# Kernel tuning notes

Measured on AMD Instinct MI355X. Metric: run time of the kernel, lower is better.

## Reference

```python
import jax, jax.numpy as jnp
import numpy as np


def setup_inputs() -> dict:
    key = jax.random.key(0)
    ks = jax.random.split(key, 7)
    B, N, D = 32, 512, 64
    H = D // 2
    return {
        "receiver": jax.random.normal(ks[0], (B, N, D), dtype=jnp.float32),
        "attendant": jax.random.normal(ks[1], (B, N, D), dtype=jnp.float32),
        "adj_mask": jax.random.uniform(ks[2], (B, N, N), dtype=jnp.float32),
        "w_q": jax.random.normal(ks[3], (D, H), dtype=jnp.float32) * (1.0 / np.sqrt(D)),
        "w_k": jax.random.normal(ks[4], (D, H), dtype=jnp.float32) * (1.0 / np.sqrt(D)),
        "bias": jax.random.normal(ks[5], (H,), dtype=jnp.float32) * 0.1,
        "a": jax.random.normal(ks[6], (H,), dtype=jnp.float32) * 0.1,
    }


def reference(receiver, attendant, adj_mask, w_q, w_k, bias, a):
    # keys: [B,N,H], queries: [B,N,H]
    keys = receiver @ w_k
    queries = attendant @ w_q
    # additive (GAT-style) scores: broadcast-add -> tanh -> dot with a
    # e_act: [B, N, M, H]  (N from keys, M from queries, matching torch unsqueeze(-3)/(-2))
    e_act = jnp.tanh(queries[:, None, :, :] + keys[:, :, None, :] + bias)
    e_scores = jnp.einsum("bnmh,h->bnm", e_act, a)
    # masked projection: adj @ scores @ adj
    att = jnp.einsum("bnk,bkm->bnm", adj_mask, e_scores)
    att = jnp.einsum("bnk,bkm->bnm", att, adj_mask)
    return att
```

## Files before the change

kernel.cpp:

```cpp
#include <hip/hip_runtime.h>

#define GN 512
#define HH 32
#define DD 64

typedef float v4f __attribute__((ext_vector_type(4)));
typedef unsigned int v4u __attribute__((ext_vector_type(4)));
typedef u_int32_t u32;
typedef u32 v2u __attribute__((ext_vector_type(2)));
typedef __bf16 v8bf __attribute__((ext_vector_type(8)));

__device__ __forceinline__ u32 f2bf(float f) {
  u32 u = __builtin_bit_cast(u32, f);
  return (u + 0x7fffu + ((u >> 16) & 1u)) >> 16;
}
__device__ __forceinline__ u32 pack2(float a, float b) {
  return f2bf(a) | (f2bf(b) << 16);
}

#define GLOAD16(g, l)                                                              \
  __builtin_amdgcn_global_load_lds((const __attribute__((address_space(1))) u32*)(g), \
                                   (__attribute__((address_space(3))) u32*)(l), 16, 0, 0)
#define VMCNT0 asm volatile("s_waitcnt vmcnt(0)" ::: "memory")

__global__ __launch_bounds__(256) void kq_kernel(const float* __restrict__ rec,
                                                 const float* __restrict__ att,
                                                 const float* __restrict__ wq,
                                                 const float* __restrict__ wk,
                                                 const float* __restrict__ bias,
                                                 float* __restrict__ ekbuf,
                                                 float* __restrict__ eqbuf) {
  __shared__ float rr[512], ra[512];
  int tid = threadIdx.x;
  size_t base = (size_t)blockIdx.x * 8;
  const float* gr = rec + base * DD;
  const float* ga = att + base * DD;
  rr[tid] = gr[tid]; rr[tid + 256] = gr[tid + 256];
  ra[tid] = ga[tid]; ra[tid + 256] = ga[tid + 256];
  __syncthreads();
  int r = tid >> 5, h = tid & 31;
  float sk = bias[h], sq = 0.f;
  const float* rrow = &rr[r * DD];
  const float* arow = &ra[r * DD];
#pragma unroll 8
  for (int d = 0; d < DD; ++d) {
    sk += rrow[d] * wk[d * HH + h];
    sq += arow[d] * wq[d * HH + h];
  }
  const float C = 2.8853900817779268f;
  ekbuf[(base + r) * HH + h] = __builtin_exp2f(C * sk);
  eqbuf[(base + r) * HH + h] = __builtin_exp2f(C * sq);
}

__global__ __launch_bounds__(256) void prep2_kernel(const float* __restrict__ adj,
                                                    const float* __restrict__ ek,
                                                    const float* __restrict__ eq,
                                                    const float* __restrict__ avec,
                                                    unsigned short* __restrict__ adjT,
                                                    unsigned short* __restrict__ adjBF,
                                                    unsigned short* __restrict__ Et) {
  __shared__ __align__(16) float smem[4608];
  int tid = threadIdx.x;
  int bid = blockIdx.x;
  int type = bid % 5, grp = bid / 5;

  if (type < 4) {
    float (*klt)[68] = (float (*)[68])smem;
    float (*ql)[36] = (float (*)[36])&smem[2176];
    int e = grp * 4 + type;
    int b = e >> 6, rem = e & 63;
    int n0 = (rem & 7) * 64, m0 = (rem >> 3) * 64;

    const float* kb = ek + ((size_t)b * GN + n0) * HH;
    const float* qb = eq + ((size_t)b * GN + m0) * HH;
    int sr = tid >> 3, sp = tid & 7;
    v4f rk0 = *(const v4f*)(kb + sr * HH + sp * 4);
    v4f rq0 = *(const v4f*)(qb + sr * HH + sp * 4);
    v4f rk1 = *(const v4f*)(kb + (sr + 32) * HH + sp * 4);
    v4f rq1 = *(const v4f*)(qb + (sr + 32) * HH + sp * 4);
    *(v4f*)&ql[sr][sp * 4] = rq0;
    *(v4f*)&ql[sr + 32][sp * 4] = rq1;
#pragma unroll
    for (int ee = 0; ee < 4; ++ee) {
      klt[sp * 4 + ee][sr] = rk0[ee];
      klt[sp * 4 + ee][sr + 32] = rk1[ee];
    }

    float a2s[HH];
    float asum = 0.f;
#pragma unroll
    for (int h = 0; h < HH; ++h) {
      float av = avec[h];
      a2s[h] = 2.0f * av;
      asum += av;
    }
    __syncthreads();

    int mg = tid >> 4, ng = tid & 15;
    v4f acc[4];
#pragma unroll
    for (int i = 0; i < 4; ++i) acc[i] = (v4f){0.f, 0.f, 0.f, 0.f};

#pragma unroll
    for (int h4 = 0; h4 < 8; ++h4) {
      v4f kv[4], qv[4];
#pragma unroll
      for (int ee = 0; ee < 4; ++ee) kv[ee] = *(const v4f*)&klt[h4 * 4 + ee][4 * ng];
#pragma unroll
      for (int i = 0; i < 4; ++i) qv[i] = *(const v4f*)&ql[mg + 16 * i][h4 * 4];
      float a0 = a2s[h4 * 4 + 0], a1 = a2s[h4 * 4 + 1];
      float a2 = a2s[h4 * 4 + 2], a3 = a2s[h4 * 4 + 3];
#pragma unroll
      for (int i = 0; i < 4; ++i) {
        v4f f0 = kv[0] * qv[i][0] + 1.0f;
        v4f f1 = kv[1] * qv[i][1] + 1.0f;
        v4f f2 = kv[2] * qv[i][2] + 1.0f;
        v4f f3 = kv[3] * qv[i][3] + 1.0f;
        v4f den0 = f0 * f1, den1 = f2 * f3;
        v4f num0 = a0 * f1 + a1 * f0;
        v4f num1 = a2 * f3 + a3 * f2;
        v4f r0, r1;
#pragma unroll
        for (int ee = 0; ee < 4; ++ee) {
          r0[ee] = __builtin_amdgcn_rcpf(den0[ee]);
          r1[ee] = __builtin_amdgcn_rcpf(den1[ee]);
        }
        acc[i] += num0 * r0;
        acc[i] += num1 * r1;
      }
    }
#pragma unroll
    for (int i = 0; i < 4; ++i) {
      v4f s = asum - acc[i];
      v2u p = {pack2(s[0], s[1]), pack2(s[2], s[3])};
      *(v2u*)(Et + ((size_t)b * GN + m0 + mg + 16 * i) * GN + n0 + 4 * ng) = p;
    }
  } else {
    float (*t)[65] = (float (*)[65])smem;
#pragma unroll 1
    for (int l = 0; l < 4; ++l) {
      int tt = grp * 4 + l;
      int b = tt >> 6, rem = tt & 63;
      int c0 = (rem & 7) * 64, r0 = (rem >> 3) * 64;
      const float* ab = adj + (size_t)b * GN * GN;
      unsigned short* ob = adjT + (size_t)b * GN * GN;
      unsigned short* of = adjBF + (size_t)b * GN * GN;
#pragma unroll
      for (int k = 0; k < 4; ++k) {
        int v = tid + k * 256;
        int row = v >> 4, seg = v & 15;
        v4f f = *(const v4f*)(ab + (size_t)(r0 + row) * GN + c0 + seg * 4);
        t[row][seg * 4 + 0] = f[0];
        t[row][seg * 4 + 1] = f[1];
        t[row][seg * 4 + 2] = f[2];
        t[row][seg * 4 + 3] = f[3];
        v2u p = {pack2(f[0], f[1]), pack2(f[2], f[3])};
        *(v2u*)(of + (size_t)(r0 + row) * GN + c0 + seg * 4) = p;
      }
      __syncthreads();
      {
        int c = tid >> 2;
        int rs = (tid & 3) * 16;
        v4u p0, p1;
#pragma unroll
        for (int j = 0; j < 4; ++j) {
          p0[j] = pack2(t[rs + 2 * j][c], t[rs + 2 * j + 1][c]);
          p1[j] = pack2(t[rs + 8 + 2 * j][c], t[rs + 9 + 2 * j][c]);
        }
        unsigned short* dst = ob + (size_t)(c0 + c) * GN + r0 + rs;
        *(v4u*)dst = p0;
        *(v4u*)(dst + 8) = p1;
      }
      __syncthreads();
    }
  }
}

#define SWZ(r, s) ((s) ^ ((r) & 7))

template <bool OUTF32>
__global__ __launch_bounds__(256) void gemm_bt(const unsigned short* __restrict__ A,
                                               const unsigned short* __restrict__ Bt,
                                               void* __restrict__ Cv) {
  __shared__ unsigned short At[2][128 * 64];
  __shared__ unsigned short Bs[2][128 * 64];
  int bid = blockIdx.x;
  int swz = (bid & 7) * 64 + (bid >> 3);
  int b = swz >> 4;
  int row0 = ((swz >> 2) & 3) * 128;
  int col0 = (swz & 3) * 128;
  int tid = threadIdx.x, lane = tid & 63, wave = tid >> 6;
  int wr = wave >> 1, wc = wave & 1;
  const unsigned short* Ab = A + (size_t)b * GN * GN;
  const unsigned short* Bb = Bt + (size_t)b * GN * GN;

  v4f acc[4][4];
#pragma unroll
  for (int i = 0; i < 4; ++i)
#pragma unroll
    for (int j = 0; j < 4; ++j) acc[i][j] = (v4f){0.f, 0.f, 0.f, 0.f};

  int cc_r[4], cc_s[4];
#pragma unroll
  for (int i = 0; i < 4; ++i) {
    int c = i * 256 + tid;
    cc_r[i] = c >> 3;
    cc_s[i] = SWZ(c >> 3, c & 7);
  }

#define STAGE(buf, kt)                                                                   \
  {                                                                                      \
    _Pragma("unroll") for (int i = 0; i < 4; ++i) {                                      \
      const unsigned short* ga = Ab + (size_t)(row0 + cc_r[i]) * GN + (kt)*64 + cc_s[i] * 8; \
      const unsigned short* gb = Bb + (size_t)(col0 + cc_r[i]) * GN + (kt)*64 + cc_s[i] * 8; \
      GLOAD16(ga, (char*)&At[buf][0] + (i * 256 + wave * 64) * 16);                      \
      GLOAD16(gb, (char*)&Bs[buf][0] + (i * 256 + wave * 64) * 16);                      \
    }                                                                                    \
  }

#define COMPUTE(buf)                                                                     \
  {                                                                                      \
    int lr = lane & 15, s16 = lane >> 4;                                                 \
    _Pragma("unroll") for (int h = 0; h < 2; ++h) {                                      \
      int sl = h * 4 + s16;                                                              \
      v8bf af[4], bfv[4];                                                                \
      _Pragma("unroll") for (int i = 0; i < 4; ++i) {                                    \
        int r = wr * 64 + i * 16 + lr;                                                   \
        af[i] = *(const v8bf*)&At[buf][r * 64 + SWZ(r, sl) * 8];                         \
      }                                                                                  \
      _Pragma("unroll") for (int j = 0; j < 4; ++j) {                                    \
        int r = wc * 64 + j * 16 + lr;                                                   \
        bfv[j] = *(const v8bf*)&Bs[buf][r * 64 + SWZ(r, sl) * 8];                        \
      }                                                                                  \
      _Pragma("unroll") for (int i = 0; i < 4; ++i)                                      \
          _Pragma("unroll") for (int j = 0; j < 4; ++j) acc[i][j] =                      \
          __builtin_amdgcn_mfma_f32_16x16x32_bf16(af[i], bfv[j], acc[i][j], 0, 0, 0);    \
    }                                                                                    \
  }

  STAGE(0, 0);
  VMCNT0;
  __builtin_amdgcn_s_barrier();
#pragma unroll
  for (int kt = 0; kt < 7; ++kt) {
    int cur = kt & 1;
    STAGE(cur ^ 1, kt + 1);
    COMPUTE(cur);
    VMCNT0;
    __builtin_amdgcn_s_barrier();
  }
  COMPUTE(1);

  int lc = lane & 15;
  int lrow4 = (lane >> 4) * 4;
#pragma unroll
  for (int i = 0; i < 4; ++i) {
#pragma unroll
    for (int j = 0; j < 4; ++j) {
      int gr = row0 + wr * 64 + i * 16 + lrow4;
      int gc = col0 + wc * 64 + j * 16 + lc;
#pragma unroll
      for (int e = 0; e < 4; ++e) {
        float v = acc[i][j][e];
        if constexpr (OUTF32)
          ((float*)Cv)[(size_t)b * GN * GN + (size_t)(gr + e) * GN + gc] = v;
        else
          ((unsigned short*)Cv)[(size_t)b * GN * GN + (size_t)(gr + e) * GN + gc] =
              (unsigned short)f2bf(v);
      }
    }
  }
#undef STAGE
#undef COMPUTE
}

extern "C" void kernel_launch(void* const* d_in, const int* in_sizes, int n_in,
                              void* d_out, int out_size, void* d_ws, size_t ws_size,
                              hipStream_t stream) {
  const float* receiver  = (const float*)d_in[0];
  const float* attendant = (const float*)d_in[1];
  const float* adj       = (const float*)d_in[2];
  const float* wq        = (const float*)d_in[3];
  const float* wk        = (const float*)d_in[4];
  const float* bias      = (const float*)d_in[5];
  const float* avec      = (const float*)d_in[6];
  float* out = (float*)d_out;

  char* ws = (char*)d_ws;
  float* ekbuf          = (float*)(ws);
  float* eqbuf          = (float*)(ws + (2u << 20));
  unsigned short* Et    = (unsigned short*)(ws + (4u << 20));
  unsigned short* adjT  = (unsigned short*)(ws + (20u << 20));
  unsigned short* adjBF = (unsigned short*)(ws + (36u << 20));
  unsigned short* Tbuf  = (unsigned short*)(ws + (52u << 20));

  kq_kernel<<<dim3(2048), dim3(256), 0, stream>>>(receiver, attendant, wq, wk, bias,
                                                  ekbuf, eqbuf);
  prep2_kernel<<<dim3(2560), dim3(256), 0, stream>>>(adj, ekbuf, eqbuf, avec,
                                                     adjT, adjBF, Et);
  gemm_bt<false><<<dim3(512), dim3(256), 0, stream>>>(adjBF, Et, Tbuf);
  gemm_bt<true><<<dim3(512), dim3(256), 0, stream>>>(Tbuf, adjT, out);
}
```

Before: 76.17 us.

## Switch GEMM to K=32 tiles with 4-stage LDS prefetch pipeline

The bf16 batched GEMM now uses K-tiles of 32 instead of 64, with four LDS buffers and three tiles in flight. Partial vmcnt waits keep loads outstanding across iterations instead of draining the queue every step, and the swizzle is adapted to 4-chunk rows. This should hide global-load latency better, at the cost of twice as many barriers and smaller compute per iteration.

```diff
diff --git a/kernel.cpp b/kernel.cpp
--- a/kernel.cpp
+++ b/kernel.cpp
@@ -176,14 +176,13 @@
   }
 }
 
-#define SWZ(r, s) ((s) ^ ((r) & 7))
+#define SWZ32(r, s) ((s) ^ (((r) >> 1) & 3))
 
 template <bool OUTF32>
 __global__ __launch_bounds__(256) void gemm_bt(const unsigned short* __restrict__ A,
                                                const unsigned short* __restrict__ Bt,
                                                void* __restrict__ Cv) {
-  __shared__ unsigned short At[2][128 * 64];
-  __shared__ unsigned short Bs[2][128 * 64];
+  __shared__ unsigned short lds[4][8192];
   int bid = blockIdx.x;
   int swz = (bid & 7) * 64 + (bid >> 3);
   int b = swz >> 4;
@@ -200,56 +199,53 @@
 #pragma unroll
     for (int j = 0; j < 4; ++j) acc[i][j] = (v4f){0.f, 0.f, 0.f, 0.f};
 
-  int cc_r[4], cc_s[4];
-#pragma unroll
-  for (int i = 0; i < 4; ++i) {
-    int c = i * 256 + tid;
-    cc_r[i] = c >> 3;
-    cc_s[i] = SWZ(c >> 3, c & 7);
-  }
+  int r0c = tid >> 2, s0c = SWZ32(tid >> 2, tid & 3);
+  int r1c = (tid + 256) >> 2, s1c = SWZ32((tid + 256) >> 2, tid & 3);
 
 #define STAGE(buf, kt)                                                                   \
   {                                                                                      \
-    _Pragma("unroll") for (int i = 0; i < 4; ++i) {                                      \
-      const unsigned short* ga = Ab + (size_t)(row0 + cc_r[i]) * GN + (kt)*64 + cc_s[i] * 8; \
-      const unsigned short* gb = Bb + (size_t)(col0 + cc_r[i]) * GN + (kt)*64 + cc_s[i] * 8; \
-      GLOAD16(ga, (char*)&At[buf][0] + (i * 256 + wave * 64) * 16);                      \
-      GLOAD16(gb, (char*)&Bs[buf][0] + (i * 256 + wave * 64) * 16);                      \
-    }                                                                                    \
+    GLOAD16(Ab + (size_t)(row0 + r0c) * GN + (kt)*32 + s0c * 8,                          \
+            (char*)&lds[buf][0] + (wave * 64) * 16);                                     \
+    GLOAD16(Ab + (size_t)(row0 + r1c) * GN + (kt)*32 + s1c * 8,                          \
+            (char*)&lds[buf][0] + (256 + wave * 64) * 16);                               \
+    GLOAD16(Bb + (size_t)(col0 + r0c) * GN + (kt)*32 + s0c * 8,                          \
+            (char*)&lds[buf][4096] + (wave * 64) * 16);                                  \
+    GLOAD16(Bb + (size_t)(col0 + r1c) * GN + (kt)*32 + s1c * 8,                          \
+            (char*)&lds[buf][4096] + (256 + wave * 64) * 16);                            \
   }
 
 #define COMPUTE(buf)                                                                     \
   {                                                                                      \
     int lr = lane & 15, s16 = lane >> 4;                                                 \
-    _Pragma("unroll") for (int h = 0; h < 2; ++h) {                                      \
-      int sl = h * 4 + s16;                                                              \
-      v8bf af[4], bfv[4];                                                                \
-      _Pragma("unroll") for (int i = 0; i < 4; ++i) {                                    \
-        int r = wr * 64 + i * 16 + lr;                                                   \
-        af[i] = *(const v8bf*)&At[buf][r * 64 + SWZ(r, sl) * 8];                         \
-      }                                                                                  \
-      _Pragma("unroll") for (int j = 0; j < 4; ++j) {                                    \
-        int r = wc * 64 + j * 16 + lr;                                                   \
-        bfv[j] = *(const v8bf*)&Bs[buf][r * 64 + SWZ(r, sl) * 8];                        \
-      }                                                                                  \
-      _Pragma("unroll") for (int i = 0; i < 4; ++i)                                      \
-          _Pragma("unroll") for (int j = 0; j < 4; ++j) acc[i][j] =                      \
-          __builtin_amdgcn_mfma_f32_16x16x32_bf16(af[i], bfv[j], acc[i][j], 0, 0, 0);    \
+    v8bf af[4], bfv[4];                                                                  \
+    _Pragma("unroll") for (int i = 0; i < 4; ++i) {                                      \
+      int r = wr * 64 + i * 16 + lr;                                                     \
+      af[i] = *(const v8bf*)&lds[buf][r * 32 + SWZ32(r, s16) * 8];                       \
     }                                                                                    \
+    _Pragma("unroll") for (int j = 0; j < 4; ++j) {                                      \
+      int r = wc * 64 + j * 16 + lr;                                                     \
+      bfv[j] = *(const v8bf*)&lds[buf][4096 + r * 32 + SWZ32(r, s16) * 8];               \
+    }                                                                                    \
+    _Pragma("unroll") for (int i = 0; i < 4; ++i)                                        \
+        _Pragma("unroll") for (int j = 0; j < 4; ++j) acc[i][j] =                        \
+        __builtin_amdgcn_mfma_f32_16x16x32_bf16(af[i], bfv[j], acc[i][j], 0, 0, 0);      \
   }
 
   STAGE(0, 0);
-  VMCNT0;
-  __builtin_amdgcn_s_barrier();
-#pragma unroll
-  for (int kt = 0; kt < 7; ++kt) {
-    int cur = kt & 1;
-    STAGE(cur ^ 1, kt + 1);
-    COMPUTE(cur);
-    VMCNT0;
+  STAGE(1, 1);
+  STAGE(2, 2);
+#pragma unroll
+  for (int kt = 0; kt < 16; ++kt) {
+    if (kt <= 13)
+      asm volatile("s_waitcnt vmcnt(8)" ::: "memory");
+    else if (kt == 14)
+      asm volatile("s_waitcnt vmcnt(4)" ::: "memory");
+    else
+      VMCNT0;
     __builtin_amdgcn_s_barrier();
-  }
-  COMPUTE(1);
+    if (kt + 3 < 16) STAGE((kt + 3) & 3, kt + 3);
+    COMPUTE(kt & 3);
+  }
 
   int lc = lane & 15;
   int lrow4 = (lane >> 4) * 4;
```

Measured after the change: 77.23 us. No clear change (+1.4%).

## Merge reciprocal pairs in score loop and prefetch adjacency tiles in transpose path

Applied to the files above, without the earlier changes.

In the score kernel, the two rational terms per four-element group are now combined over a common denominator, so each element needs one reciprocal instead of two, at the cost of a few extra multiplies. In the adjacency conversion and transpose branch, the four tile iterations are software-pipelined with two register buffers. The global loads for the next tile are issued before the current tile is processed, so load latency overlaps the shared-memory transpose and stores. This raises register use and risks overflow or precision loss in the larger product denominator.

```diff
diff --git a/kernel.cpp b/kernel.cpp
--- a/kernel.cpp
+++ b/kernel.cpp
@@ -116,17 +116,15 @@
         v4f f1 = kv[1] * qv[i][1] + 1.0f;
         v4f f2 = kv[2] * qv[i][2] + 1.0f;
         v4f f3 = kv[3] * qv[i][3] + 1.0f;
-        v4f den0 = f0 * f1, den1 = f2 * f3;
-        v4f num0 = a0 * f1 + a1 * f0;
-        v4f num1 = a2 * f3 + a3 * f2;
-        v4f r0, r1;
-#pragma unroll
-        for (int ee = 0; ee < 4; ++ee) {
-          r0[ee] = __builtin_amdgcn_rcpf(den0[ee]);
-          r1[ee] = __builtin_amdgcn_rcpf(den1[ee]);
-        }
-        acc[i] += num0 * r0;
-        acc[i] += num1 * r1;
+        v4f f01 = f0 * f1, f23 = f2 * f3;
+        v4f den = f01 * f23;
+        v4f t01 = a0 * f1 + a1 * f0;
+        v4f t23 = a2 * f3 + a3 * f2;
+        v4f num = t01 * f23 + t23 * f01;
+        v4f r;
+#pragma unroll
+        for (int ee = 0; ee < 4; ++ee) r[ee] = __builtin_amdgcn_rcpf(den[ee]);
+        acc[i] += num * r;
       }
     }
 #pragma unroll
@@ -137,42 +135,66 @@
     }
   } else {
     float (*t)[65] = (float (*)[65])smem;
-#pragma unroll 1
-    for (int l = 0; l < 4; ++l) {
-      int tt = grp * 4 + l;
-      int b = tt >> 6, rem = tt & 63;
-      int c0 = (rem & 7) * 64, r0 = (rem >> 3) * 64;
-      const float* ab = adj + (size_t)b * GN * GN;
-      unsigned short* ob = adjT + (size_t)b * GN * GN;
-      unsigned short* of = adjBF + (size_t)b * GN * GN;
-#pragma unroll
-      for (int k = 0; k < 4; ++k) {
-        int v = tid + k * 256;
-        int row = v >> 4, seg = v & 15;
-        v4f f = *(const v4f*)(ab + (size_t)(r0 + row) * GN + c0 + seg * 4);
-        t[row][seg * 4 + 0] = f[0];
-        t[row][seg * 4 + 1] = f[1];
-        t[row][seg * 4 + 2] = f[2];
-        t[row][seg * 4 + 3] = f[3];
-        v2u p = {pack2(f[0], f[1]), pack2(f[2], f[3])};
-        *(v2u*)(of + (size_t)(r0 + row) * GN + c0 + seg * 4) = p;
-      }
-      __syncthreads();
-      {
-        int c = tid >> 2;
-        int rs = (tid & 3) * 16;
-        v4u p0, p1;
-#pragma unroll
-        for (int j = 0; j < 4; ++j) {
-          p0[j] = pack2(t[rs + 2 * j][c], t[rs + 2 * j + 1][c]);
-          p1[j] = pack2(t[rs + 8 + 2 * j][c], t[rs + 9 + 2 * j][c]);
-        }
-        unsigned short* dst = ob + (size_t)(c0 + c) * GN + r0 + rs;
-        *(v4u*)dst = p0;
-        *(v4u*)(dst + 8) = p1;
-      }
-      __syncthreads();
-    }
+    int base_tt = grp * 4;
+    v4f ra[4], rb[4];
+
+#define TLOAD(dst, l)                                                          \
+    {                                                                          \
+      int tt = base_tt + (l);                                                  \
+      int b_ = tt >> 6, rem_ = tt & 63;                                        \
+      int c0_ = (rem_ & 7) * 64, r0_ = (rem_ >> 3) * 64;                       \
+      const float* ab_ = adj + (size_t)b_ * GN * GN;                           \
+      _Pragma("unroll") for (int k = 0; k < 4; ++k) {                          \
+        int v = tid + k * 256;                                                 \
+        int row = v >> 4, seg = v & 15;                                        \
+        dst[k] = *(const v4f*)(ab_ + (size_t)(r0_ + row) * GN + c0_ + seg * 4); \
+      }                                                                        \
+    }
+
+#define TPROCESS(src, l)                                                       \
+    {                                                                          \
+      int tt = base_tt + (l);                                                  \
+      int b_ = tt >> 6, rem_ = tt & 63;                                        \
+      int c0_ = (rem_ & 7) * 64, r0_ = (rem_ >> 3) * 64;                       \
+      unsigned short* ob_ = adjT + (size_t)b_ * GN * GN;                       \
+      unsigned short* of_ = adjBF + (size_t)b_ * GN * GN;                      \
+      _Pragma("unroll") for (int k = 0; k < 4; ++k) {                          \
+        int v = tid + k * 256;                                                 \
+        int row = v >> 4, seg = v & 15;                                        \
+        v4f f = src[k];                                                        \
+        t[row][seg * 4 + 0] = f[0];                                            \
+        t[row][seg * 4 + 1] = f[1];                                            \
+        t[row][seg * 4 + 2] = f[2];                                            \
+        t[row][seg * 4 + 3] = f[3];                                            \
+        v2u p = {pack2(f[0], f[1]), pack2(f[2], f[3])};                        \
+        *(v2u*)(of_ + (size_t)(r0_ + row) * GN + c0_ + seg * 4) = p;           \
+      }                                                                        \
+      __syncthreads();                                                         \
+      {                                                                        \
+        int c = tid >> 2;                                                      \
+        int rs = (tid & 3) * 16;                                               \
+        v4u p0, p1;                                                            \
+        _Pragma("unroll") for (int j = 0; j < 4; ++j) {                        \
+          p0[j] = pack2(t[rs + 2 * j][c], t[rs + 2 * j + 1][c]);               \
+          p1[j] = pack2(t[rs + 8 + 2 * j][c], t[rs + 9 + 2 * j][c]);           \
+        }                                                                      \
+        unsigned short* dst_ = ob_ + (size_t)(c0_ + c) * GN + r0_ + rs;        \
+        *(v4u*)dst_ = p0;                                                      \
+        *(v4u*)(dst_ + 8) = p1;                                                \
+      }                                                                        \
+      __syncthreads();                                                         \
+    }
+
+    TLOAD(ra, 0);
+    TLOAD(rb, 1);
+    TPROCESS(ra, 0);
+    TLOAD(ra, 2);
+    TPROCESS(rb, 1);
+    TLOAD(rb, 3);
+    TPROCESS(ra, 2);
+    TPROCESS(rb, 3);
+#undef TLOAD
+#undef TPROCESS
   }
 }
 
```

Measured after the change: 74.51 us (median of 2 runs). 1.02x faster.
